# Kernel tuning notes

Hardware: AMD Instinct MI355X
Metric: run time of the kernel (lower is better)

The kernel has to match this reference:

```python
import jax, jax.numpy as jnp
import numpy as np

B, T, D, H = 16, 2048, 1024, 512  # input_size D == 2*H (bidirectional, k=3 highway)


def setup_inputs() -> dict:
    key = jax.random.key(0)
    k1, k2 = jax.random.split(key, 2)
    x = jax.random.normal(k1, (B, T, D), dtype=jnp.float32)
    # W: [D, dir, H, 3] -> slices: 0 = x_tilde, 1 = f-gate preact, 2 = r-gate preact
    W = jax.random.normal(k2, (D, 2, H, 3), dtype=jnp.float32) / np.sqrt(D)
    # bias: [dir, 2, H] -> bias[:,0]=b_f, bias[:,1]=b_r
    bias = jnp.zeros((2, 2, H), dtype=jnp.float32)
    return {"x": x, "W": W, "bias": bias}


def _scan_dir(g0, f, r, xres):
    """Elementwise SRU recurrence over time. All inputs [T, B, H]."""
    def step(c, inp):
        g_t, f_t, r_t, x_t = inp
        c = f_t * c + (1.0 - f_t) * g_t
        h = r_t * jnp.tanh(c) + (1.0 - r_t) * x_t
        return c, h
    c_last, h = jax.lax.scan(step, jnp.zeros_like(g0[0]), (g0, f, r, xres))
    return h, c_last  # [T,B,H], [B,H]


def _sru(x, W, bias):
    xt = jnp.swapaxes(x, 0, 1)                      # [T, B, D]
    U = jnp.einsum('tbd,dzhk->tbzhk', xt, W)        # [T, B, dir, H, 3]
    g0 = U[..., 0]                                  # [T, B, 2, H]
    f = jax.nn.sigmoid(U[..., 1] + bias[:, 0])      # broadcast [2,H]
    r = jax.nn.sigmoid(U[..., 2] + bias[:, 1])
    xres = xt.reshape(T, B, 2, H)                   # highway residual per direction (k=3)

    # forward direction
    h_f, c_f = _scan_dir(g0[:, :, 0], f[:, :, 0], r[:, :, 0], xres[:, :, 0])
    # backward direction: flip time, scan, flip back
    h_b, c_b = _scan_dir(g0[::-1, :, 1], f[::-1, :, 1], r[::-1, :, 1], xres[::-1, :, 1])
    h_b = h_b[::-1]

    out = jnp.concatenate([h_f, h_b], axis=-1)      # [T, B, 2H]
    c_last = jnp.concatenate([c_f, c_b], axis=-1)   # [B, 2H]
    return out, c_last


def reference(x, W, bias):
    out, c_last = _sru(x, W, bias)
    # wrapper transposes back to batch-first; c: (layers=1, B, 2H) -> (B, 1, 2H)
    return jnp.swapaxes(out, 0, 1), c_last[:, None, :]
```

## Files before the change

kernel.cpp:

```cpp
#include <hip/hip_runtime.h>
#include <cstdint>

typedef unsigned int uint;
typedef unsigned short ushort;
typedef __attribute__((ext_vector_type(8))) __bf16 bf16x8;
typedef __attribute__((ext_vector_type(4))) float f32x4;
typedef __attribute__((ext_vector_type(4))) ushort us4;

#define BB 16
#define TT 2048
#define DD 1024
#define HH 512

__device__ inline ushort f2bf(float f) {
    uint u = __float_as_uint(f);
    u += 0x7FFF + ((u >> 16) & 1);
    return (ushort)(u >> 16);
}
__device__ inline float bf2f(ushort b) {
    return __uint_as_float(((uint)b) << 16);
}
__device__ inline float sigm(float x) { return 1.f / (1.f + __expf(-x)); }

__device__ inline void gload16(const void* g, void* l) {
    __builtin_amdgcn_global_load_lds(
        (const __attribute__((address_space(1))) uint*)g,
        (__attribute__((address_space(3))) uint*)l, 16, 0, 0);
}

__global__ __launch_bounds__(256) void convert_W(const float* __restrict__ W,
                                                 ushort* __restrict__ Bth,
                                                 ushort* __restrict__ Btl) {
    int idx = blockIdx.x * 256 + threadIdx.x;
    int d   = idx & 1023;
    int n   = idx >> 10;
    int z    = n / 1536;
    int rem  = n % 1536;
    int gate = rem >> 9;
    int h    = rem & 511;
    float w    = W[(size_t)d * 3072 + z * 1536 + h * 3 + gate];
    ushort whi = f2bf(w);
    Bth[idx]   = whi;
    Btl[idx]   = f2bf(w - bf2f(whi));
}

__global__ __launch_bounds__(256, 2) void gemm_bf16split(
    const float* __restrict__ x, const ushort* __restrict__ Bth,
    const ushort* __restrict__ Btl, float* __restrict__ C) {
    __shared__ ushort lds[4 * 128 * 32];

    const int t    = threadIdx.x;
    const int w    = t >> 6;
    const int lane = t & 63;
    const size_t m0 = (size_t)blockIdx.x * 128;
    const size_t n0 = (size_t)blockIdx.y * 128;
    const int wm = w >> 1, wn = w & 1;

    f32x4 acc[4][4];
#pragma unroll
    for (int i = 0; i < 4; i++)
#pragma unroll
        for (int j = 0; j < 4; j++) acc[i][j] = (f32x4)(0.f);

    const int srow  = w * 32 + (lane >> 2);
    const int kphys = lane & 3;

    const int frow  = lane & 15;
    const int fkoff = (((lane >> 4) ^ ((frow >> 1) & 3)) << 3);

    for (int k0 = 0; k0 < 1024; k0 += 32) {
        float4 xv[4];
#pragma unroll
        for (int p = 0; p < 4; p++) {
            int ridx = p * 256 + t;
            int row  = ridx >> 3;
            int kq   = ridx & 7;
            xv[p] = *(const float4*)(x + (m0 + row) * 1024 + k0 + kq * 4);
        }
#pragma unroll
        for (int arr = 0; arr < 2; arr++) {
            const ushort* G = arr ? Btl : Bth;
#pragma unroll
            for (int c = 0; c < 2; c++) {
                const int row = srow + c * 16;
                const int kcl = kphys ^ ((row >> 1) & 3);
                const ushort* src = G + ((n0 + row) << 10) + k0 + (kcl << 3);
                char* dst = (char*)lds + (2 + arr) * 8192 +
                            (w * 32 + c * 16) * 64 + lane * 16;
                gload16(src, dst);
            }
        }
#pragma unroll
        for (int p = 0; p < 4; p++) {
            int ridx = p * 256 + t;
            int row  = ridx >> 3;
            int kq   = ridx & 7;
            int off  = row * 64 + (((kq >> 1) ^ ((row >> 1) & 3)) << 4) +
                       ((kq & 1) << 3);
            float vf[4] = {xv[p].x, xv[p].y, xv[p].z, xv[p].w};
            us4 hi, lo;
#pragma unroll
            for (int j = 0; j < 4; j++) {
                ushort h = f2bf(vf[j]);
                hi[j]    = h;
                lo[j]    = f2bf(vf[j] - bf2f(h));
            }
            *(us4*)((char*)lds + off)        = hi;
            *(us4*)((char*)lds + 8192 + off) = lo;
        }
        __syncthreads();

        bf16x8 fa[4], fal[4], fb[4], fbl[4];
#pragma unroll
        for (int i = 0; i < 4; i++) {
            const int ra = (wm * 64 + i * 16 + frow) * 32;
            const int rb = (wn * 64 + i * 16 + frow) * 32;
            fa[i]  = *(const bf16x8*)&lds[0 * 4096 + ra + fkoff];
            fal[i] = *(const bf16x8*)&lds[1 * 4096 + ra + fkoff];
            fb[i]  = *(const bf16x8*)&lds[2 * 4096 + rb + fkoff];
            fbl[i] = *(const bf16x8*)&lds[3 * 4096 + rb + fkoff];
        }
#pragma unroll
        for (int i = 0; i < 4; i++)
#pragma unroll
            for (int j = 0; j < 4; j++) {
                acc[i][j] = __builtin_amdgcn_mfma_f32_16x16x32_bf16(
                    fa[i], fb[j], acc[i][j], 0, 0, 0);
                acc[i][j] = __builtin_amdgcn_mfma_f32_16x16x32_bf16(
                    fa[i], fbl[j], acc[i][j], 0, 0, 0);
                acc[i][j] = __builtin_amdgcn_mfma_f32_16x16x32_bf16(
                    fal[i], fb[j], acc[i][j], 0, 0, 0);
            }
        __syncthreads();
    }

    const int ccol = lane & 15;
    const int crow = (lane >> 4) * 4;
#pragma unroll
    for (int i = 0; i < 4; i++) {
        const size_t mrow = m0 + wm * 64 + i * 16 + crow;
#pragma unroll
        for (int j = 0; j < 4; j++) {
            const size_t ncol = n0 + wn * 64 + j * 16 + ccol;
            float* Cp = C + mrow * 3072 + ncol;
#pragma unroll
            for (int r = 0; r < 4; r++) Cp[(size_t)r * 3072] = acc[i][j][r];
        }
    }
}

#define SCH 16384
#define NCH 16
#define CL 128

__global__ __launch_bounds__(256) void scanA(const float* __restrict__ U,
                                             const float* __restrict__ bias,
                                             float* __restrict__ F,
                                             float* __restrict__ Cp) {
    int idx = blockIdx.x * 256 + threadIdx.x;
    int ch  = idx & (SCH - 1);
    int s   = idx >> 14;
    int b = ch >> 10, z = (ch >> 9) & 1, h = ch & 511;
    float bf = bias[z * 1024 + h];
    const float* Ub = U + (size_t)b * TT * 3072 + z * 1536 + h;
    float c = 0.f, Fa = 1.f;
    for (int q = 0; q < CL; q++) {
        int n = s * CL + q;
        int t = z ? (TT - 1 - n) : n;
        size_t o = (size_t)t * 3072;
        float g = Ub[o], fp = Ub[o + 512];
        float f = sigm(fp + bf);
        c  = f * c + (1.f - f) * g;
        Fa *= f;
    }
    F[s * SCH + ch]  = Fa;
    Cp[s * SCH + ch] = c;
}

__global__ __launch_bounds__(256) void scanB(const float* __restrict__ F,
                                             const float* __restrict__ Cp,
                                             float* __restrict__ cstart) {
    int ch = blockIdx.x * 256 + threadIdx.x;
    float c = 0.f;
    for (int s = 0; s < NCH; s++) {
        cstart[s * SCH + ch] = c;
        c = F[s * SCH + ch] * c + Cp[s * SCH + ch];
    }
}

__global__ __launch_bounds__(256) void scanC(const float* __restrict__ U,
                                             const float* __restrict__ x,
                                             const float* __restrict__ bias,
                                             const float* __restrict__ cstart,
                                             float* __restrict__ out) {
    int idx = blockIdx.x * 256 + threadIdx.x;
    int ch  = idx & (SCH - 1);
    int s   = idx >> 14;
    int b = ch >> 10, z = (ch >> 9) & 1, h = ch & 511;
    float bf = bias[z * 1024 + h];
    float br = bias[z * 1024 + 512 + h];
    const float* Ub = U + (size_t)b * TT * 3072 + z * 1536 + h;
    const float* xb = x + (size_t)b * TT * 1024 + z * 512 + h;
    float* ob       = out + (size_t)b * TT * 1024 + z * 512 + h;
    float c = cstart[s * SCH + ch];
    for (int q = 0; q < CL; q++) {
        int n = s * CL + q;
        int t = z ? (TT - 1 - n) : n;
        size_t o = (size_t)t * 3072;
        float g = Ub[o], fp = Ub[o + 512], rp = Ub[o + 1024];
        float xv = xb[(size_t)t * 1024];
        float f = sigm(fp + bf);
        float r = sigm(rp + br);
        c = f * c + (1.f - f) * g;
        float e  = __expf(2.f * c);
        float th = 1.f - 2.f / (e + 1.f);
        ob[(size_t)t * 1024] = r * th + (1.f - r) * xv;
    }
    if (s == NCH - 1)
        out[(size_t)BB * TT * 1024 + b * 1024 + z * 512 + h] = c;
}

extern "C" void kernel_launch(void* const* d_in, const int* in_sizes, int n_in,
                              void* d_out, int out_size, void* d_ws,
                              size_t ws_size, hipStream_t stream) {
    const float* x    = (const float*)d_in[0];
    const float* W    = (const float*)d_in[1];
    const float* bias = (const float*)d_in[2];
    float* out        = (float*)d_out;

    char* ws    = (char*)d_ws;
    float* U    = (float*)ws;
    ushort* Bth = (ushort*)(ws + 402653184UL);
    ushort* Btl = (ushort*)(ws + 408944640UL);
    float* F    = (float*)(ws + 402653184UL);
    float* Cp   = (float*)(ws + 406847488UL);
    float* cst  = (float*)(ws + 411041792UL);

    convert_W<<<12288, 256, 0, stream>>>(W, Bth, Btl);

    dim3 grid(256, 24);
    gemm_bf16split<<<grid, 256, 0, stream>>>(x, Bth, Btl, U);

    scanA<<<1024, 256, 0, stream>>>(U, bias, F, Cp);
    scanB<<<64, 256, 0, stream>>>(F, Cp, cst);
    scanC<<<1024, 256, 0, stream>>>(U, x, bias, cst, out);
}
```

Baseline: 1.016 ms.

## Prefetch GEMM x tiles across iterations and vectorize scan kernels with float4

```diff
diff --git a/kernel.cpp b/kernel.cpp
--- a/kernel.cpp
+++ b/kernel.cpp
@@ -21,6 +21,7 @@
     return __uint_as_float(((uint)b) << 16);
 }
 __device__ inline float sigm(float x) { return 1.f / (1.f + __expf(-x)); }
+__device__ inline float4 ld4(const float* p) { return *(const float4*)p; }
 
 __device__ inline void gload16(const void* g, void* l) {
     __builtin_amdgcn_global_load_lds(
@@ -64,19 +65,19 @@
 
     const int srow  = w * 32 + (lane >> 2);
     const int kphys = lane & 3;
-
     const int frow  = lane & 15;
     const int fkoff = (((lane >> 4) ^ ((frow >> 1) & 3)) << 3);
 
+    float4 xv[4];
+#pragma unroll
+    for (int p = 0; p < 4; p++) {
+        int ridx = p * 256 + t;
+        int row  = ridx >> 3;
+        int kq   = ridx & 7;
+        xv[p] = ld4(x + (m0 + row) * 1024 + kq * 4);
+    }
+
     for (int k0 = 0; k0 < 1024; k0 += 32) {
-        float4 xv[4];
-#pragma unroll
-        for (int p = 0; p < 4; p++) {
-            int ridx = p * 256 + t;
-            int row  = ridx >> 3;
-            int kq   = ridx & 7;
-            xv[p] = *(const float4*)(x + (m0 + row) * 1024 + k0 + kq * 4);
-        }
 #pragma unroll
         for (int arr = 0; arr < 2; arr++) {
             const ushort* G = arr ? Btl : Bth;
@@ -120,6 +121,17 @@
             fb[i]  = *(const bf16x8*)&lds[2 * 4096 + rb + fkoff];
             fbl[i] = *(const bf16x8*)&lds[3 * 4096 + rb + fkoff];
         }
+
+        const int k0n = (k0 + 32) & 1023;
+        float4 xn[4];
+#pragma unroll
+        for (int p = 0; p < 4; p++) {
+            int ridx = p * 256 + t;
+            int row  = ridx >> 3;
+            int kq   = ridx & 7;
+            xn[p] = ld4(x + (m0 + row) * 1024 + k0n + kq * 4);
+        }
+
 #pragma unroll
         for (int i = 0; i < 4; i++)
 #pragma unroll
@@ -132,6 +144,8 @@
                     fal[i], fb[j], acc[i][j], 0, 0, 0);
             }
         __syncthreads();
+#pragma unroll
+        for (int p = 0; p < 4; p++) xv[p] = xn[p];
     }
 
     const int ccol = lane & 15;
@@ -150,41 +164,68 @@
 }
 
 #define SCH 16384
-#define NCH 16
-#define CL 128
+#define NCH 32
+#define CL 64
+
+#define STEPA(CC, FA, G, FP, BF)          \
+    {                                     \
+        float ff = sigm((FP) + (BF));     \
+        CC = ff * CC + (1.f - ff) * (G);  \
+        FA *= ff;                         \
+    }
+
+#define STEPC(CC, G, FP, RP, XV, BF, BR, OUT)       \
+    {                                               \
+        float ff = sigm((FP) + (BF));               \
+        float rr = sigm((RP) + (BR));               \
+        CC = ff * CC + (1.f - ff) * (G);            \
+        float e  = __expf(2.f * CC);                \
+        float th = 1.f - 2.f / (e + 1.f);           \
+        OUT = rr * th + (1.f - rr) * (XV);          \
+    }
 
 __global__ __launch_bounds__(256) void scanA(const float* __restrict__ U,
                                              const float* __restrict__ bias,
                                              float* __restrict__ F,
                                              float* __restrict__ Cp) {
-    int idx = blockIdx.x * 256 + threadIdx.x;
-    int ch  = idx & (SCH - 1);
-    int s   = idx >> 14;
-    int b = ch >> 10, z = (ch >> 9) & 1, h = ch & 511;
-    float bf = bias[z * 1024 + h];
-    const float* Ub = U + (size_t)b * TT * 3072 + z * 1536 + h;
-    float c = 0.f, Fa = 1.f;
+    int tid = blockIdx.x * 256 + threadIdx.x;
+    int s   = tid >> 12;
+    int ci  = tid & 4095;
+    int b = ci >> 8, z = (ci >> 7) & 1, h4 = (ci & 127) << 2;
+    float4 bf = ld4(&bias[z * 1024 + h4]);
+    const float* Ub = U + (size_t)b * TT * 3072 + z * 1536 + h4;
+    float4 c  = {0.f, 0.f, 0.f, 0.f};
+    float4 Fa = {1.f, 1.f, 1.f, 1.f};
+#pragma unroll 4
     for (int q = 0; q < CL; q++) {
         int n = s * CL + q;
         int t = z ? (TT - 1 - n) : n;
         size_t o = (size_t)t * 3072;
-        float g = Ub[o], fp = Ub[o + 512];
-        float f = sigm(fp + bf);
-        c  = f * c + (1.f - f) * g;
-        Fa *= f;
-    }
-    F[s * SCH + ch]  = Fa;
-    Cp[s * SCH + ch] = c;
+        float4 g = ld4(Ub + o);
+        float4 f = ld4(Ub + o + 512);
+        STEPA(c.x, Fa.x, g.x, f.x, bf.x);
+        STEPA(c.y, Fa.y, g.y, f.y, bf.y);
+        STEPA(c.z, Fa.z, g.z, f.z, bf.z);
+        STEPA(c.w, Fa.w, g.w, f.w, bf.w);
+    }
+    *(float4*)&F[((size_t)s << 14) + (ci << 2)]  = Fa;
+    *(float4*)&Cp[((size_t)s << 14) + (ci << 2)] = c;
 }
 
 __global__ __launch_bounds__(256) void scanB(const float* __restrict__ F,
                                              const float* __restrict__ Cp,
                                              float* __restrict__ cstart) {
-    int ch = blockIdx.x * 256 + threadIdx.x;
-    float c = 0.f;
+    int ci = blockIdx.x * 256 + threadIdx.x;
+    float4 c = {0.f, 0.f, 0.f, 0.f};
     for (int s = 0; s < NCH; s++) {
-        cstart[s * SCH + ch] = c;
-        c = F[s * SCH + ch] * c + Cp[s * SCH + ch];
+        size_t o = ((size_t)s << 14) + (ci << 2);
+        *(float4*)&cstart[o] = c;
+        float4 Fv = ld4(&F[o]);
+        float4 Cv = ld4(&Cp[o]);
+        c.x = Fv.x * c.x + Cv.x;
+        c.y = Fv.y * c.y + Cv.y;
+        c.z = Fv.z * c.z + Cv.z;
+        c.w = Fv.w * c.w + Cv.w;
     }
 }
 
@@ -193,31 +234,34 @@
                                              const float* __restrict__ bias,
                                              const float* __restrict__ cstart,
                                              float* __restrict__ out) {
-    int idx = blockIdx.x * 256 + threadIdx.x;
-    int ch  = idx & (SCH - 1);
-    int s   = idx >> 14;
-    int b = ch >> 10, z = (ch >> 9) & 1, h = ch & 511;
-    float bf = bias[z * 1024 + h];
-    float br = bias[z * 1024 + 512 + h];
-    const float* Ub = U + (size_t)b * TT * 3072 + z * 1536 + h;
-    const float* xb = x + (size_t)b * TT * 1024 + z * 512 + h;
-    float* ob       = out + (size_t)b * TT * 1024 + z * 512 + h;
-    float c = cstart[s * SCH + ch];
+    int tid = blockIdx.x * 256 + threadIdx.x;
+    int s   = tid >> 12;
+    int ci  = tid & 4095;
+    int b = ci >> 8, z = (ci >> 7) & 1, h4 = (ci & 127) << 2;
+    float4 bf = ld4(&bias[z * 1024 + h4]);
+    float4 br = ld4(&bias[z * 1024 + 512 + h4]);
+    const float* Ub = U + (size_t)b * TT * 3072 + z * 1536 + h4;
+    const float* xb = x + (size_t)b * TT * 1024 + z * 512 + h4;
+    float* ob       = out + (size_t)b * TT * 1024 + z * 512 + h4;
+    float4 c = ld4(&cstart[((size_t)s << 14) + (ci << 2)]);
+#pragma unroll 2
     for (int q = 0; q < CL; q++) {
         int n = s * CL + q;
         int t = z ? (TT - 1 - n) : n;
         size_t o = (size_t)t * 3072;
-        float g = Ub[o], fp = Ub[o + 512], rp = Ub[o + 1024];
-        float xv = xb[(size_t)t * 1024];
-        float f = sigm(fp + bf);
-        float r = sigm(rp + br);
-        c = f * c + (1.f - f) * g;
-        float e  = __expf(2.f * c);
-        float th = 1.f - 2.f / (e + 1.f);
-        ob[(size_t)t * 1024] = r * th + (1.f - r) * xv;
+        float4 g  = ld4(Ub + o);
+        float4 f  = ld4(Ub + o + 512);
+        float4 r  = ld4(Ub + o + 1024);
+        float4 xv = ld4(xb + (size_t)t * 1024);
+        float4 hv;
+        STEPC(c.x, g.x, f.x, r.x, xv.x, bf.x, br.x, hv.x);
+        STEPC(c.y, g.y, f.y, r.y, xv.y, bf.y, br.y, hv.y);
+        STEPC(c.z, g.z, f.z, r.z, xv.z, bf.z, br.z, hv.z);
+        STEPC(c.w, g.w, f.w, r.w, xv.w, bf.w, br.w, hv.w);
+        *(float4*)(ob + (size_t)t * 1024) = hv;
     }
     if (s == NCH - 1)
-        out[(size_t)BB * TT * 1024 + b * 1024 + z * 512 + h] = c;
+        *(float4*)(out + (size_t)BB * TT * 1024 + b * 1024 + z * 512 + h4) = c;
 }
 
 extern "C" void kernel_launch(void* const* d_in, const int* in_sizes, int n_in,
@@ -233,15 +277,15 @@
     ushort* Bth = (ushort*)(ws + 402653184UL);
     ushort* Btl = (ushort*)(ws + 408944640UL);
     float* F    = (float*)(ws + 402653184UL);
-    float* Cp   = (float*)(ws + 406847488UL);
-    float* cst  = (float*)(ws + 411041792UL);
+    float* Cp   = (float*)(ws + 404750336UL);
+    float* cst  = (float*)(ws + 406847488UL);
 
     convert_W<<<12288, 256, 0, stream>>>(W, Bth, Btl);
 
     dim3 grid(256, 24);
     gemm_bf16split<<<grid, 256, 0, stream>>>(x, Bth, Btl, U);
 
-    scanA<<<1024, 256, 0, stream>>>(U, bias, F, Cp);
-    scanB<<<64, 256, 0, stream>>>(F, Cp, cst);
-    scanC<<<1024, 256, 0, stream>>>(U, x, bias, cst, out);
-}
+    scanA<<<512, 256, 0, stream>>>(U, bias, F, Cp);
+    scanB<<<16, 256, 0, stream>>>(F, Cp, cst);
+    scanC<<<512, 256, 0, stream>>>(U, x, bias, cst, out);
+}
```

New measurement: 1.017 ms. No clear change (+0.2%).
